# Kernel tuning notes

Hardware: AMD Instinct MI355X
Metric: run time of the kernel (lower is better)

## Reference

```python
import jax, jax.numpy as jnp
import numpy as np

B, T, N, V, C, E = 64, 100, 25, 128, 128, 64
EPS = 1e-5


def setup_inputs() -> dict:
    key = jax.random.key(0)
    ks = jax.random.split(key, 6)
    x = jax.random.normal(ks[0], (B, T, N, V), jnp.float32)
    edge_index = jax.random.randint(ks[1], (2, E), 0, N, dtype=jnp.int64)
    W1 = jax.random.normal(ks[2], (V, C), jnp.float32) * (1.0 / np.sqrt(V))
    b1 = jnp.zeros((C,), jnp.float32)
    W2 = jax.random.normal(ks[3], (C, C), jnp.float32) * (1.0 / np.sqrt(C))
    b2 = jnp.zeros((C,), jnp.float32)
    gamma = jnp.ones((T,), jnp.float32)
    beta = jnp.zeros((T,), jnp.float32)
    return {"x": x, "edge_index": edge_index, "W1": W1, "b1": b1,
            "W2": W2, "b2": b2, "gamma": gamma, "beta": beta}


def _gcn_norm(edge_index, n):
    # GCNConv default: add self-loops, symmetric D^{-1/2} A_hat D^{-1/2} norm.
    loop = jnp.arange(n, dtype=edge_index.dtype)
    src = jnp.concatenate([edge_index[0], loop])  # [E + N]
    tgt = jnp.concatenate([edge_index[1], loop])
    deg = jnp.zeros((n,), jnp.float32).at[tgt].add(1.0)
    dis = jax.lax.rsqrt(deg)  # deg >= 1 due to self-loops
    return src, tgt, dis[src] * dis[tgt]


def _gcn_layer(h, W, b, src, tgt, norm):
    # h: [G, N, Cin] -> [G, N, Cout]; linear then gather-scale-scatter aggregate.
    h = jnp.einsum('gnc,cd->gnd', h, W)
    msg = h[:, src, :] * norm[None, :, None]          # [G, E+N, Cout]
    out = jnp.zeros_like(h).at[:, tgt, :].add(msg)    # scatter-add to targets
    return out + b


def reference(x, edge_index, W1, b1, W2, b2, gamma, beta):
    Bv, Tv, Nv, Vv = x.shape
    h = x.reshape(Bv * Tv, Nv, Vv)  # B*T independent graphs, shared edge_index
    src, tgt, norm = _gcn_norm(edge_index, Nv)
    h = _gcn_layer(h, W1, b1, src, tgt, norm)
    h = _gcn_layer(h, W2, b2, src, tgt, norm)
    y = h.reshape(Bv, Tv, Nv, -1)
    # BatchNorm2d(T) in training mode: batch stats over (B, N, C) per T-channel.
    mean = y.mean(axis=(0, 2, 3), keepdims=True)
    var = y.var(axis=(0, 2, 3), keepdims=True)  # biased, matches torch normalization
    y = (y - mean) * jax.lax.rsqrt(var + EPS)
    y = y * gamma[None, :, None, None] + beta[None, :, None, None]
    return jax.nn.relu(y)
```

## Files before the change

### kernel.cpp

```cpp
#include <hip/hip_runtime.h>

#define T_DIM   100
#define N_NODES 25
#define C_DIM   128
#define B_DIM   64
#define G_TOTAL 6400
#define GNV     3200
#define CNT_PER_T 204800.0f

#define WS_A2P  0
#define WS_RS1  640
#define WS_BW   768
#define WS_SUM  1024
#define WS_SSQ  1152
#define WS_W12T 2048

#define YSTR  36
#define YGSTR (128 * YSTR)

typedef __attribute__((ext_vector_type(8))) short short8;
typedef __attribute__((ext_vector_type(4))) float f32x4;

__device__ __forceinline__ unsigned short f2bf(float f) {
  unsigned int u = __float_as_uint(f);
  u += 0x7FFFu + ((u >> 16) & 1u);
  return (unsigned short)(u >> 16);
}
__device__ __forceinline__ unsigned int pack2bf(float a, float b) {
  return (unsigned int)f2bf(a) | ((unsigned int)f2bf(b) << 16);
}

__global__ void k_pre(const int* __restrict__ edge, const float* __restrict__ W1,
                      const float* __restrict__ W2, const float* __restrict__ b1,
                      float* __restrict__ wsf) {
  __shared__ float sA[N_NODES * N_NODES];
  __shared__ float sA2[N_NODES * N_NODES];
  __shared__ float sdeg[N_NODES];
  __shared__ float sdis[N_NODES];
  const int tid = threadIdx.x;

  if (blockIdx.x < 64) {
    int j = blockIdx.x * 256 + tid;
    int c = j & 127, v = j >> 7;
    float acc = 0.f;
#pragma unroll 8
    for (int u = 0; u < 128; u++) acc = fmaf(W1[v * 128 + u], W2[u * 128 + c], acc);
    ((unsigned short*)(wsf + WS_W12T))[c * 128 + v] = f2bf(acc);
    if (j < 128) {
      float a2 = 0.f;
      for (int u = 0; u < 128; u++) a2 = fmaf(W2[u * 128 + j], b1[u], a2);
      wsf[WS_BW + j] = a2;
    }
    return;
  }

  if (tid < N_NODES) sdeg[tid] = 0.f;
  for (int j = tid; j < N_NODES * N_NODES; j += 256) sA[j] = 0.f;
  __syncthreads();
  if (tid < 64) atomicAdd(&sdeg[edge[64 + tid]], 1.f);
  __syncthreads();
  if (tid < N_NODES) sdis[tid] = rsqrtf(sdeg[tid] + 1.f);
  __syncthreads();
  if (tid < 64) {
    int s = edge[tid], tg = edge[64 + tid];
    atomicAdd(&sA[tg * N_NODES + s], sdis[s] * sdis[tg]);
  }
  __syncthreads();
  if (tid < N_NODES) atomicAdd(&sA[tid * N_NODES + tid], sdis[tid] * sdis[tid]);
  __syncthreads();
  for (int j = tid; j < N_NODES * N_NODES; j += 256) {
    int n = j / N_NODES, m = j - n * N_NODES;
    float acc = 0.f;
    for (int k = 0; k < N_NODES; k++) acc = fmaf(sA[n * N_NODES + k], sA[k * N_NODES + m], acc);
    sA2[j] = acc;
  }
  __syncthreads();
  for (int j = tid; j < 1024; j += 256) {
    int m = j >> 5, k = j & 31;
    float v = (m < N_NODES && k < N_NODES) ? sA2[m * N_NODES + k] : 0.f;
    ((unsigned short*)(wsf + WS_A2P))[j] = f2bf(v);
  }
  if (tid < N_NODES) {
    float rs = 0.f;
    for (int m = 0; m < N_NODES; m++) rs += sA[tid * N_NODES + m];
    wsf[WS_RS1 + tid] = rs;
  }
  if (tid < T_DIM) { wsf[WS_SUM + tid] = 0.f; wsf[WS_SSQ + tid] = 0.f; }
}

__global__ __launch_bounds__(256, 4) void k_main(const float* __restrict__ x,
                                                 const float* __restrict__ b2,
                                                 const float* __restrict__ wsc,
                                                 float* __restrict__ stats,
                                                 float* __restrict__ out) {
  __shared__ __align__(16) unsigned short LB[4 * YGSTR];
  __shared__ float sBW[128];
  __shared__ float sB2[128];
  __shared__ float rs1[32];
  __shared__ float red[8];
  const int tid = threadIdx.x;
  const int bid = blockIdx.x;
  const int t = bid % T_DIM;
  const int bq = bid / T_DIM;
  const int wv = tid >> 6, lane = tid & 63, quad = lane >> 4, l16 = lane & 15;

  if (tid < 128) {
    sBW[tid] = wsc[WS_BW + tid];
    if (tid < N_NODES) rs1[tid] = wsc[WS_RS1 + tid];
  } else {
    sB2[tid - 128] = b2[tid - 128];
  }
  for (int j = tid; j < 12 * 128; j += 256) {
    int pr = j >> 7;
    int g = pr / 3, rr = pr - (pr / 3) * 3;
    LB[(g * 28 + 25 + rr) * 128 + (j & 127)] = 0;
  }

  {
    const float* xb = x + (bq * 4 * T_DIM + t) * GNV;
    for (int idx = tid; idx < 1600; idx += 256) {
      int row = idx >> 4;
      int c8  = (idx & 15) << 3;
      int g = (row * 41) >> 10;
      int n = row - g * 25;
      const float4* xp = (const float4*)(xb + g * (T_DIM * GNV) + n * 128 + c8);
      float4 f0 = xp[0], f1 = xp[1];
      uint4 w;
      w.x = pack2bf(f0.x, f0.y); w.y = pack2bf(f0.z, f0.w);
      w.z = pack2bf(f1.x, f1.y); w.w = pack2bf(f1.z, f1.w);
      int r = g * 28 + n;
      *(uint4*)&LB[r * 128 + (c8 ^ ((r & 15) << 3))] = w;
    }
  }

  short8 bfr[2][4];
  {
    const unsigned short* Wg = (const unsigned short*)(wsc + WS_W12T);
#pragma unroll
    for (int nt = 0; nt < 2; nt++) {
      const short8* rp = (const short8*)&Wg[(wv * 32 + nt * 16 + l16) * 128];
#pragma unroll
      for (int ks = 0; ks < 4; ks++) bfr[nt][ks] = rp[(ks << 2) | quad];
    }
  }
  __syncthreads();

  f32x4 acc[7][2];
#pragma unroll
  for (int mt = 0; mt < 7; mt++)
#pragma unroll
    for (int nt = 0; nt < 2; nt++)
#pragma unroll
      for (int r = 0; r < 4; r++) acc[mt][nt][r] = 0.f;

#pragma unroll
  for (int ks = 0; ks < 4; ks++) {
    const int cc = (ks << 2) | quad;
#pragma unroll
    for (int mt = 0; mt < 7; mt++) {
      int arow = mt * 16 + l16;
      short8 afr = *(const short8*)&LB[arow * 128 + ((cc ^ (arow & 15)) << 3)];
#pragma unroll
      for (int nt = 0; nt < 2; nt++)
        acc[mt][nt] = __builtin_amdgcn_mfma_f32_16x16x32_bf16(afr, bfr[nt][ks], acc[mt][nt], 0, 0, 0);
    }
  }
  __syncthreads();

#pragma unroll
  for (int mt = 0; mt < 7; mt++) {
    int row0 = mt * 16 + quad * 4;
    int g = row0 / 28;
    int rl = row0 - g * 28;
#pragma unroll
    for (int nt = 0; nt < 2; nt++) {
      int c = wv * 32 + nt * 16 + l16;
      uint2 p;
      p.x = pack2bf(acc[mt][nt][0], acc[mt][nt][1]);
      p.y = pack2bf(acc[mt][nt][2], acc[mt][nt][3]);
      *(uint2*)&LB[g * YGSTR + c * YSTR + rl] = p;
    }
  }
  {
    uint2 z; z.x = 0u; z.y = 0u;
    for (int j = tid; j < 512; j += 256) {
      int g = j >> 7, c = j & 127;
      *(uint2*)&LB[g * YGSTR + c * YSTR + 28] = z;
    }
  }
  __syncthreads();

  const unsigned short* A2p = (const unsigned short*)(wsc + WS_A2P);
  short8 a2f[2];
#pragma unroll
  for (int mt2 = 0; mt2 < 2; mt2++)
    a2f[mt2] = *(const short8*)&A2p[(mt2 * 16 + l16) * 32 + quad * 8];

  const int obase = ((bq * 4 + wv) * T_DIM + t) * GNV;
  float sum = 0.f, ssq = 0.f;
#pragma unroll
  for (int half = 0; half < 2; half++) {
    f32x4 acc2[2][4];
#pragma unroll
    for (int mt2 = 0; mt2 < 2; mt2++)
#pragma unroll
      for (int nt = 0; nt < 4; nt++)
#pragma unroll
        for (int r = 0; r < 4; r++) acc2[mt2][nt][r] = 0.f;

#pragma unroll
    for (int nt = 0; nt < 4; nt++) {
      int c = (half * 4 + nt) * 16 + l16;
      int base = wv * YGSTR + c * YSTR + quad * 8;
      uint2 lo = *(const uint2*)&LB[base];
      uint2 hi = *(const uint2*)&LB[base + 4];
      uint4 w; w.x = lo.x; w.y = lo.y; w.z = hi.x; w.w = hi.y;
      short8 bf = __builtin_bit_cast(short8, w);
#pragma unroll
      for (int mt2 = 0; mt2 < 2; mt2++)
        acc2[mt2][nt] = __builtin_amdgcn_mfma_f32_16x16x32_bf16(a2f[mt2], bf, acc2[mt2][nt], 0, 0, 0);
    }
#pragma unroll
    for (int mt2 = 0; mt2 < 2; mt2++) {
#pragma unroll
      for (int nt = 0; nt < 4; nt++) {
        int c = (half * 4 + nt) * 16 + l16;
        float bw = sBW[c], bb = sB2[c];
#pragma unroll
        for (int r = 0; r < 4; r++) {
          int m = mt2 * 16 + quad * 4 + r;
          if (m < N_NODES) {
            float v = acc2[mt2][nt][r] + rs1[m] * bw + bb;
            out[obase + m * 128 + c] = v;
            sum += v;
            ssq += v * v;
          }
        }
      }
    }
  }

#pragma unroll
  for (int off = 32; off > 0; off >>= 1) {
    sum += __shfl_down(sum, off, 64);
    ssq += __shfl_down(ssq, off, 64);
  }
  if (lane == 0) { red[wv] = sum; red[4 + wv] = ssq; }
  __syncthreads();
  if (tid == 0) {
    atomicAdd(&stats[t], red[0] + red[1] + red[2] + red[3]);
    atomicAdd(&stats[128 + t], red[4] + red[5] + red[6] + red[7]);
  }
}

#define NORM_STR  1280000
__global__ __launch_bounds__(256) void k_norm(float* __restrict__ out,
                                              const float* __restrict__ stats,
                                              const float* __restrict__ gamma,
                                              const float* __restrict__ beta) {
  const int i0 = blockIdx.x * 256 + threadIdx.x;
  const float inv = 1.f / CNT_PER_T;
  float4 h[4];
  float g[4], bb[4];
  int base[4];
#pragma unroll
  for (int k = 0; k < 4; k++) {
    int i4 = i0 + k * NORM_STR;
    base[k] = i4 * 4;
    int t = (base[k] / GNV) % T_DIM;
    float s = stats[t], q = stats[128 + t];
    float mean = s * inv;
    float var = fmaf(q, inv, -mean * mean);
    float rstd = rsqrtf(var + 1e-5f);
    g[k] = gamma[t] * rstd;
    bb[k] = fmaf(-mean, g[k], beta[t]);
    h[k] = *(const float4*)(out + base[k]);
  }
#pragma unroll
  for (int k = 0; k < 4; k++) {
    float4 v = h[k];
    v.x = fmaxf(fmaf(v.x, g[k], bb[k]), 0.f);
    v.y = fmaxf(fmaf(v.y, g[k], bb[k]), 0.f);
    v.z = fmaxf(fmaf(v.z, g[k], bb[k]), 0.f);
    v.w = fmaxf(fmaf(v.w, g[k], bb[k]), 0.f);
    *(float4*)(out + base[k]) = v;
  }
}

extern "C" void kernel_launch(void* const* d_in, const int* in_sizes, int n_in,
                              void* d_out, int out_size, void* d_ws, size_t ws_size,
                              hipStream_t stream) {
  const float* x     = (const float*)d_in[0];
  const int*   edge  = (const int*)d_in[1];
  const float* W1    = (const float*)d_in[2];
  const float* b1    = (const float*)d_in[3];
  const float* W2    = (const float*)d_in[4];
  const float* b2    = (const float*)d_in[5];
  const float* gamma = (const float*)d_in[6];
  const float* beta  = (const float*)d_in[7];
  float* out = (float*)d_out;
  float* wsf = (float*)d_ws;

  k_pre<<<65, 256, 0, stream>>>(edge, W1, W2, b1, wsf);
  k_main<<<G_TOTAL / 4, 256, 0, stream>>>(x, b2, wsf, wsf + WS_SUM, out);
  k_norm<<<NORM_STR / 256, 256, 0, stream>>>(out, wsf + WS_SUM, gamma, beta);
}
```

Before: 205.6 us.

## Fuse main GCN and batchnorm kernels via persistent grid with per-T completion counters

Replaces the separate main and normalize kernels with one persistent kernel of 800 blocks. Each block processes two chunks, publishes its partial sums per T, then spin-waits until all 16 contributors for its T are done before normalizing its own output region. The aim is to drop one kernel launch and have the normalize pass read output that is likely still in cache. The spin-wait relies on all 800 blocks being co-resident (256 CUs times 4 blocks per CU), so a launch that cannot fit them all risks deadlock.

```diff
diff --git a/kernel.cpp b/kernel.cpp
--- a/kernel.cpp
+++ b/kernel.cpp
@@ -3,17 +3,16 @@
 #define T_DIM   100
 #define N_NODES 25
 #define C_DIM   128
-#define B_DIM   64
-#define G_TOTAL 6400
 #define GNV     3200
 #define CNT_PER_T 204800.0f
+#define GRID_MAIN 800
 
 #define WS_A2P  0
 #define WS_RS1  640
 #define WS_BW   768
-#define WS_SUM  1024
-#define WS_SSQ  1152
 #define WS_W12T 2048
+#define WS_PART 10240
+#define WS_CNT  13440
 
 #define YSTR  36
 #define YGSTR (128 * YSTR)
@@ -85,57 +84,35 @@
     for (int m = 0; m < N_NODES; m++) rs += sA[tid * N_NODES + m];
     wsf[WS_RS1 + tid] = rs;
   }
-  if (tid < T_DIM) { wsf[WS_SUM + tid] = 0.f; wsf[WS_SSQ + tid] = 0.f; }
-}
-
-__global__ __launch_bounds__(256, 4) void k_main(const float* __restrict__ x,
-                                                 const float* __restrict__ b2,
-                                                 const float* __restrict__ wsc,
-                                                 float* __restrict__ stats,
-                                                 float* __restrict__ out) {
+  if (tid < T_DIM)
+    __hip_atomic_store((unsigned int*)(wsf + WS_CNT) + tid, 0u,
+                       __ATOMIC_RELEASE, __HIP_MEMORY_SCOPE_AGENT);
+}
+
+__global__ __launch_bounds__(256, 4) void k_mainnorm(
+    const float* __restrict__ x, const float* __restrict__ b2,
+    const float* __restrict__ gamma, const float* __restrict__ beta,
+    float* __restrict__ wsf, float* __restrict__ out) {
   __shared__ __align__(16) unsigned short LB[4 * YGSTR];
   __shared__ float sBW[128];
   __shared__ float sB2[128];
   __shared__ float rs1[32];
   __shared__ float red[8];
+  __shared__ float sred[2];
   const int tid = threadIdx.x;
   const int bid = blockIdx.x;
-  const int t = bid % T_DIM;
-  const int bq = bid / T_DIM;
   const int wv = tid >> 6, lane = tid & 63, quad = lane >> 4, l16 = lane & 15;
 
   if (tid < 128) {
-    sBW[tid] = wsc[WS_BW + tid];
-    if (tid < N_NODES) rs1[tid] = wsc[WS_RS1 + tid];
+    sBW[tid] = wsf[WS_BW + tid];
+    if (tid < N_NODES) rs1[tid] = wsf[WS_RS1 + tid];
   } else {
     sB2[tid - 128] = b2[tid - 128];
   }
-  for (int j = tid; j < 12 * 128; j += 256) {
-    int pr = j >> 7;
-    int g = pr / 3, rr = pr - (pr / 3) * 3;
-    LB[(g * 28 + 25 + rr) * 128 + (j & 127)] = 0;
-  }
-
-  {
-    const float* xb = x + (bq * 4 * T_DIM + t) * GNV;
-    for (int idx = tid; idx < 1600; idx += 256) {
-      int row = idx >> 4;
-      int c8  = (idx & 15) << 3;
-      int g = (row * 41) >> 10;
-      int n = row - g * 25;
-      const float4* xp = (const float4*)(xb + g * (T_DIM * GNV) + n * 128 + c8);
-      float4 f0 = xp[0], f1 = xp[1];
-      uint4 w;
-      w.x = pack2bf(f0.x, f0.y); w.y = pack2bf(f0.z, f0.w);
-      w.z = pack2bf(f1.x, f1.y); w.w = pack2bf(f1.z, f1.w);
-      int r = g * 28 + n;
-      *(uint4*)&LB[r * 128 + (c8 ^ ((r & 15) << 3))] = w;
-    }
-  }
 
   short8 bfr[2][4];
   {
-    const unsigned short* Wg = (const unsigned short*)(wsc + WS_W12T);
+    const unsigned short* Wg = (const unsigned short*)(wsf + WS_W12T);
 #pragma unroll
     for (int nt = 0; nt < 2; nt++) {
       const short8* rp = (const short8*)&Wg[(wv * 32 + nt * 16 + l16) * 128];
@@ -143,147 +120,191 @@
       for (int ks = 0; ks < 4; ks++) bfr[nt][ks] = rp[(ks << 2) | quad];
     }
   }
-  __syncthreads();
-
-  f32x4 acc[7][2];
-#pragma unroll
-  for (int mt = 0; mt < 7; mt++)
-#pragma unroll
-    for (int nt = 0; nt < 2; nt++)
-#pragma unroll
-      for (int r = 0; r < 4; r++) acc[mt][nt][r] = 0.f;
-
-#pragma unroll
-  for (int ks = 0; ks < 4; ks++) {
-    const int cc = (ks << 2) | quad;
-#pragma unroll
-    for (int mt = 0; mt < 7; mt++) {
-      int arow = mt * 16 + l16;
-      short8 afr = *(const short8*)&LB[arow * 128 + ((cc ^ (arow & 15)) << 3)];
-#pragma unroll
-      for (int nt = 0; nt < 2; nt++)
-        acc[mt][nt] = __builtin_amdgcn_mfma_f32_16x16x32_bf16(afr, bfr[nt][ks], acc[mt][nt], 0, 0, 0);
-    }
-  }
-  __syncthreads();
-
-#pragma unroll
-  for (int mt = 0; mt < 7; mt++) {
-    int row0 = mt * 16 + quad * 4;
-    int g = row0 / 28;
-    int rl = row0 - g * 28;
-#pragma unroll
-    for (int nt = 0; nt < 2; nt++) {
-      int c = wv * 32 + nt * 16 + l16;
-      uint2 p;
-      p.x = pack2bf(acc[mt][nt][0], acc[mt][nt][1]);
-      p.y = pack2bf(acc[mt][nt][2], acc[mt][nt][3]);
-      *(uint2*)&LB[g * YGSTR + c * YSTR + rl] = p;
-    }
-  }
-  {
-    uint2 z; z.x = 0u; z.y = 0u;
-    for (int j = tid; j < 512; j += 256) {
-      int g = j >> 7, c = j & 127;
-      *(uint2*)&LB[g * YGSTR + c * YSTR + 28] = z;
-    }
-  }
-  __syncthreads();
-
-  const unsigned short* A2p = (const unsigned short*)(wsc + WS_A2P);
+  const unsigned short* A2p = (const unsigned short*)(wsf + WS_A2P);
   short8 a2f[2];
 #pragma unroll
   for (int mt2 = 0; mt2 < 2; mt2++)
     a2f[mt2] = *(const short8*)&A2p[(mt2 * 16 + l16) * 32 + quad * 8];
 
-  const int obase = ((bq * 4 + wv) * T_DIM + t) * GNV;
-  float sum = 0.f, ssq = 0.f;
-#pragma unroll
-  for (int half = 0; half < 2; half++) {
-    f32x4 acc2[2][4];
-#pragma unroll
-    for (int mt2 = 0; mt2 < 2; mt2++)
-#pragma unroll
-      for (int nt = 0; nt < 4; nt++)
-#pragma unroll
-        for (int r = 0; r < 4; r++) acc2[mt2][nt][r] = 0.f;
-
-#pragma unroll
-    for (int nt = 0; nt < 4; nt++) {
-      int c = (half * 4 + nt) * 16 + l16;
-      int base = wv * YGSTR + c * YSTR + quad * 8;
-      uint2 lo = *(const uint2*)&LB[base];
-      uint2 hi = *(const uint2*)&LB[base + 4];
-      uint4 w; w.x = lo.x; w.y = lo.y; w.z = hi.x; w.w = hi.y;
-      short8 bf = __builtin_bit_cast(short8, w);
+  for (int iter = 0; iter < 2; iter++) {
+    const int chunk = bid + iter * GRID_MAIN;
+    const int t = chunk % T_DIM;
+    const int bq = chunk / T_DIM;
+    __syncthreads();
+
+    for (int j = tid; j < 12 * 128; j += 256) {
+      int pr = j >> 7;
+      int g = pr / 3, rr = pr - (pr / 3) * 3;
+      LB[(g * 28 + 25 + rr) * 128 + (j & 127)] = 0;
+    }
+
+    {
+      const float* xb = x + (bq * 4 * T_DIM + t) * GNV;
+      for (int idx = tid; idx < 1600; idx += 256) {
+        int row = idx >> 4;
+        int c8  = (idx & 15) << 3;
+        int g = (row * 41) >> 10;
+        int n = row - g * 25;
+        const float4* xp = (const float4*)(xb + g * (T_DIM * GNV) + n * 128 + c8);
+        float4 f0 = xp[0], f1 = xp[1];
+        uint4 w;
+        w.x = pack2bf(f0.x, f0.y); w.y = pack2bf(f0.z, f0.w);
+        w.z = pack2bf(f1.x, f1.y); w.w = pack2bf(f1.z, f1.w);
+        int r = g * 28 + n;
+        *(uint4*)&LB[r * 128 + (c8 ^ ((r & 15) << 3))] = w;
+      }
+    }
+    __syncthreads();
+
+    f32x4 acc[7][2];
+#pragma unroll
+    for (int mt = 0; mt < 7; mt++)
+#pragma unroll
+      for (int nt = 0; nt < 2; nt++)
+#pragma unroll
+        for (int r = 0; r < 4; r++) acc[mt][nt][r] = 0.f;
+
+#pragma unroll
+    for (int ks = 0; ks < 4; ks++) {
+      const int cc = (ks << 2) | quad;
+#pragma unroll
+      for (int mt = 0; mt < 7; mt++) {
+        int arow = mt * 16 + l16;
+        short8 afr = *(const short8*)&LB[arow * 128 + ((cc ^ (arow & 15)) << 3)];
+#pragma unroll
+        for (int nt = 0; nt < 2; nt++)
+          acc[mt][nt] = __builtin_amdgcn_mfma_f32_16x16x32_bf16(afr, bfr[nt][ks], acc[mt][nt], 0, 0, 0);
+      }
+    }
+    __syncthreads();
+
+#pragma unroll
+    for (int mt = 0; mt < 7; mt++) {
+      int row0 = mt * 16 + quad * 4;
+      int g = row0 / 28;
+      int rl = row0 - g * 28;
+#pragma unroll
+      for (int nt = 0; nt < 2; nt++) {
+        int c = wv * 32 + nt * 16 + l16;
+        uint2 p;
+        p.x = pack2bf(acc[mt][nt][0], acc[mt][nt][1]);
+        p.y = pack2bf(acc[mt][nt][2], acc[mt][nt][3]);
+        *(uint2*)&LB[g * YGSTR + c * YSTR + rl] = p;
+      }
+    }
+    {
+      uint2 z; z.x = 0u; z.y = 0u;
+      for (int j = tid; j < 512; j += 256) {
+        int g = j >> 7, c = j & 127;
+        *(uint2*)&LB[g * YGSTR + c * YSTR + 28] = z;
+      }
+    }
+    __syncthreads();
+
+    const int obase = ((bq * 4 + wv) * T_DIM + t) * GNV;
+    float sum = 0.f, ssq = 0.f;
+#pragma unroll
+    for (int half = 0; half < 2; half++) {
+      f32x4 acc2[2][4];
 #pragma unroll
       for (int mt2 = 0; mt2 < 2; mt2++)
-        acc2[mt2][nt] = __builtin_amdgcn_mfma_f32_16x16x32_bf16(a2f[mt2], bf, acc2[mt2][nt], 0, 0, 0);
-    }
-#pragma unroll
-    for (int mt2 = 0; mt2 < 2; mt2++) {
+#pragma unroll
+        for (int nt = 0; nt < 4; nt++)
+#pragma unroll
+          for (int r = 0; r < 4; r++) acc2[mt2][nt][r] = 0.f;
+
 #pragma unroll
       for (int nt = 0; nt < 4; nt++) {
         int c = (half * 4 + nt) * 16 + l16;
-        float bw = sBW[c], bb = sB2[c];
-#pragma unroll
-        for (int r = 0; r < 4; r++) {
-          int m = mt2 * 16 + quad * 4 + r;
-          if (m < N_NODES) {
-            float v = acc2[mt2][nt][r] + rs1[m] * bw + bb;
-            out[obase + m * 128 + c] = v;
-            sum += v;
-            ssq += v * v;
+        int base = wv * YGSTR + c * YSTR + quad * 8;
+        uint2 lo = *(const uint2*)&LB[base];
+        uint2 hi = *(const uint2*)&LB[base + 4];
+        uint4 w; w.x = lo.x; w.y = lo.y; w.z = hi.x; w.w = hi.y;
+        short8 bf = __builtin_bit_cast(short8, w);
+#pragma unroll
+        for (int mt2 = 0; mt2 < 2; mt2++)
+          acc2[mt2][nt] = __builtin_amdgcn_mfma_f32_16x16x32_bf16(a2f[mt2], bf, acc2[mt2][nt], 0, 0, 0);
+      }
+#pragma unroll
+      for (int mt2 = 0; mt2 < 2; mt2++) {
+#pragma unroll
+        for (int nt = 0; nt < 4; nt++) {
+          int c = (half * 4 + nt) * 16 + l16;
+          float bw = sBW[c], bb = sB2[c];
+#pragma unroll
+          for (int r = 0; r < 4; r++) {
+            int m = mt2 * 16 + quad * 4 + r;
+            if (m < N_NODES) {
+              float v = acc2[mt2][nt][r] + rs1[m] * bw + bb;
+              out[obase + m * 128 + c] = v;
+              sum += v;
+              ssq += v * v;
+            }
           }
         }
       }
     }
-  }
-
-#pragma unroll
-  for (int off = 32; off > 0; off >>= 1) {
-    sum += __shfl_down(sum, off, 64);
-    ssq += __shfl_down(ssq, off, 64);
-  }
-  if (lane == 0) { red[wv] = sum; red[4 + wv] = ssq; }
-  __syncthreads();
-  if (tid == 0) {
-    atomicAdd(&stats[t], red[0] + red[1] + red[2] + red[3]);
-    atomicAdd(&stats[128 + t], red[4] + red[5] + red[6] + red[7]);
-  }
-}
-
-#define NORM_STR  1280000
-__global__ __launch_bounds__(256) void k_norm(float* __restrict__ out,
-                                              const float* __restrict__ stats,
-                                              const float* __restrict__ gamma,
-                                              const float* __restrict__ beta) {
-  const int i0 = blockIdx.x * 256 + threadIdx.x;
-  const float inv = 1.f / CNT_PER_T;
-  float4 h[4];
-  float g[4], bb[4];
-  int base[4];
-#pragma unroll
-  for (int k = 0; k < 4; k++) {
-    int i4 = i0 + k * NORM_STR;
-    base[k] = i4 * 4;
-    int t = (base[k] / GNV) % T_DIM;
-    float s = stats[t], q = stats[128 + t];
-    float mean = s * inv;
-    float var = fmaf(q, inv, -mean * mean);
+
+#pragma unroll
+    for (int off = 32; off > 0; off >>= 1) {
+      sum += __shfl_down(sum, off, 64);
+      ssq += __shfl_down(ssq, off, 64);
+    }
+    if (lane == 0) { red[wv] = sum; red[4 + wv] = ssq; }
+    __syncthreads();
+    if (tid == 0) {
+      float bs = red[0] + red[1] + red[2] + red[3];
+      float bsq = red[4] + red[5] + red[6] + red[7];
+      float* part = wsf + WS_PART;
+      __hip_atomic_store(&part[t * 16 + bq], bs,
+                         __ATOMIC_RELAXED, __HIP_MEMORY_SCOPE_AGENT);
+      __hip_atomic_store(&part[1600 + t * 16 + bq], bsq,
+                         __ATOMIC_RELAXED, __HIP_MEMORY_SCOPE_AGENT);
+      __hip_atomic_fetch_add((unsigned int*)(wsf + WS_CNT) + t, 1u,
+                             __ATOMIC_RELEASE, __HIP_MEMORY_SCOPE_AGENT);
+    }
+  }
+
+  {
+    const int tn = bid % T_DIM;
+    if (tid == 0) {
+      unsigned int* cnt = (unsigned int*)(wsf + WS_CNT) + tn;
+      while (__hip_atomic_load(cnt, __ATOMIC_ACQUIRE, __HIP_MEMORY_SCOPE_AGENT) < 16u)
+        __builtin_amdgcn_s_sleep(1);
+    }
+    __syncthreads();
+    if (tid < 32) {
+      const float* pp = wsf + WS_PART + (tid < 16 ? 0 : 1600) + tn * 16 + (tid & 15);
+      float v = __hip_atomic_load(pp, __ATOMIC_RELAXED, __HIP_MEMORY_SCOPE_AGENT);
+      v += __shfl_xor(v, 8, 64);
+      v += __shfl_xor(v, 4, 64);
+      v += __shfl_xor(v, 2, 64);
+      v += __shfl_xor(v, 1, 64);
+      if ((tid & 15) == 0) sred[tid >> 4] = v;
+    }
+    __syncthreads();
+    const float inv = 1.f / CNT_PER_T;
+    float mean = sred[0] * inv;
+    float var = fmaf(sred[1], inv, -mean * mean);
     float rstd = rsqrtf(var + 1e-5f);
-    g[k] = gamma[t] * rstd;
-    bb[k] = fmaf(-mean, g[k], beta[t]);
-    h[k] = *(const float4*)(out + base[k]);
-  }
-#pragma unroll
-  for (int k = 0; k < 4; k++) {
-    float4 v = h[k];
-    v.x = fmaxf(fmaf(v.x, g[k], bb[k]), 0.f);
-    v.y = fmaxf(fmaf(v.y, g[k], bb[k]), 0.f);
-    v.z = fmaxf(fmaf(v.z, g[k], bb[k]), 0.f);
-    v.w = fmaxf(fmaf(v.w, g[k], bb[k]), 0.f);
-    *(float4*)(out + base[k]) = v;
+    float gm = gamma[tn] * rstd;
+    float bt = fmaf(-mean, gm, beta[tn]);
+#pragma unroll
+    for (int it = 0; it < 2; it++) {
+      int bq2 = (bid + it * GRID_MAIN) / T_DIM;
+#pragma unroll
+      for (int gl = 0; gl < 4; gl++) {
+        float* p = out + ((bq2 * 4 + gl) * T_DIM + tn) * GNV;
+        for (int j = tid; j < GNV / 4; j += 256) {
+          float4 v = *(const float4*)(p + 4 * j);
+          v.x = fmaxf(fmaf(v.x, gm, bt), 0.f);
+          v.y = fmaxf(fmaf(v.y, gm, bt), 0.f);
+          v.z = fmaxf(fmaf(v.z, gm, bt), 0.f);
+          v.w = fmaxf(fmaf(v.w, gm, bt), 0.f);
+          *(float4*)(p + 4 * j) = v;
+        }
+      }
+    }
   }
 }
 
@@ -302,6 +323,5 @@
   float* wsf = (float*)d_ws;
 
   k_pre<<<65, 256, 0, stream>>>(edge, W1, W2, b1, wsf);
-  k_main<<<G_TOTAL / 4, 256, 0, stream>>>(x, b2, wsf, wsf + WS_SUM, out);
-  k_norm<<<NORM_STR / 256, 256, 0, stream>>>(out, wsf + WS_SUM, gamma, beta);
-}
+  k_mainnorm<<<GRID_MAIN, 256, 0, stream>>>(x, b2, gamma, beta, wsf, out);
+}
```

Measured after the change: 359.3 us. 74.8% more time.
